# Kernel optimization log

Measured on AMD Instinct MI355X. Metric: run time of the kernel, lower is better.

The kernel has to match this reference:

```python
import jax, jax.numpy as jnp
import numpy as np

INF = 1e9  # large finite sentinel (avoid inf arithmetic in potentials)


def _hungarian(cost):
    """Exact linear sum assignment (Jonker-Volgenant style shortest augmenting
    path, O(N^3)) on a single [N, N] cost matrix. Returns col_ind (int32 [N])
    such that row i is matched to column col_ind[i] with minimal total cost
    (same solution as scipy.optimize.linear_sum_assignment up to ties).
    Column index n is a virtual 'start' column (e-maxx formulation)."""
    n = cost.shape[0]

    def row_body(i, carry):
        u, v, p = carry  # u: row potentials [n]; v: col potentials [n+1]; p[j]: row assigned to col j (-1 free)
        p = p.at[n].set(i)
        state = (u, v, p,
                 jnp.full(n + 1, INF, cost.dtype),   # minv
                 jnp.zeros(n + 1, dtype=bool),       # used
                 jnp.zeros(n + 1, dtype=jnp.int32),  # way (parent col on path)
                 jnp.int32(n))                       # j0 current col

        def cond(st):
            _, _, p_, _, _, _, j0 = st
            return p_[j0] >= 0  # stop when we reach a free column

        def body(st):
            u_, v_, p_, minv, used, way, j0 = st
            used = used.at[j0].set(True)
            i0 = p_[j0]
            cur = cost[i0] - u_[i0] - v_[:n]          # reduced costs of row i0 [n]
            cur = jnp.where(used[:n], INF, cur)
            better = cur < minv[:n]
            minv = minv.at[:n].set(jnp.where(better, cur, minv[:n]))
            way = way.at[:n].set(jnp.where(better, j0, way[:n]))
            masked = jnp.where(used[:n], INF, minv[:n])
            j1 = jnp.argmin(masked).astype(jnp.int32)
            delta = masked[j1]
            # dual update: used cols raise row potential, others shrink minv
            u_ = u_.at[p_].add(jnp.where(used, delta, jnp.zeros((), cost.dtype)))
            v_ = jnp.where(used, v_ - delta, v_)
            minv = jnp.where(used, minv, minv - delta)
            return (u_, v_, p_, minv, used, way, j1)

        u, v, p, _, _, way, j0 = jax.lax.while_loop(cond, body, state)

        # augment along the alternating path back to the virtual column
        def cond2(s):
            j, _ = s
            return j != n

        def body2(s):
            j, p_ = s
            j_prev = way[j]
            return j_prev, p_.at[j].set(p_[j_prev])

        _, p = jax.lax.while_loop(cond2, body2, (j0, p))
        return (u, v, p)

    u0 = jnp.zeros(n, cost.dtype)
    v0 = jnp.zeros(n + 1, cost.dtype)
    p0 = jnp.full(n + 1, -1, dtype=jnp.int32)
    _, _, p = jax.lax.fori_loop(0, n, row_body, (u0, v0, p0))
    # p[j] = row matched to col j  ->  col_ind[row] = j
    col_ind = jnp.zeros(n, jnp.int32).at[p[:n]].set(jnp.arange(n, dtype=jnp.int32))
    return col_ind


def setup_inputs() -> dict:
    key = jax.random.key(0)
    k1, k2 = jax.random.split(key)
    B, N, D = 2048, 24, 256
    slots = jax.random.normal(k1, (B, N, D), dtype=jnp.float32)
    prev_slots = jax.random.normal(k2, (B, N, D), dtype=jnp.float32)
    return {"slots": slots, "prev_slots": prev_slots}


def reference(slots, prev_slots):
    """HungarianPredictor.forward with similarity='cosine': reorder current
    slots to align with prev_slots ordering via optimal 1-1 matching."""
    eps = 1e-12  # torch F.normalize eps
    pn = prev_slots / jnp.maximum(
        jnp.linalg.norm(prev_slots, axis=-1, keepdims=True), eps)
    cn = slots / jnp.maximum(
        jnp.linalg.norm(slots, axis=-1, keepdims=True), eps)
    # cost[b, i, j] = 1 - <prev_i, curr_j>   [B, N, N]
    cost = 1.0 - jnp.einsum('bnd,bmd->bnm', pn, cn)
    col = jax.vmap(_hungarian)(jax.lax.stop_gradient(cost))  # [B, N] int32
    reordered = jax.vmap(lambda s, c: s[c])(slots, col)       # gather per batch
    return reordered
```

## Files before the change

### kernel.cpp

```cpp
#include <hip/hip_runtime.h>
#include <math.h>

#define N    24
#define D    256
#define BLK  256
#define NB   4
#define CTS  28
#define INFV 1e9f

__device__ __forceinline__ int readlane_i(int x, int l) {
    return __builtin_amdgcn_readlane(x, l);
}
__device__ __forceinline__ float readlane_f(float x, int l) {
    return __uint_as_float((unsigned)__builtin_amdgcn_readlane((int)__float_as_uint(x), l));
}

__device__ __forceinline__ unsigned wave_min32(unsigned x) {
    unsigned t;
    t = (unsigned)__builtin_amdgcn_update_dpp((int)x, (int)x, 0xB1,  0xF, 0xF, false); x = t < x ? t : x;
    t = (unsigned)__builtin_amdgcn_update_dpp((int)x, (int)x, 0x4E,  0xF, 0xF, false); x = t < x ? t : x;
    t = (unsigned)__builtin_amdgcn_update_dpp((int)x, (int)x, 0x114, 0xF, 0xF, false); x = t < x ? t : x;
    t = (unsigned)__builtin_amdgcn_update_dpp((int)x, (int)x, 0x118, 0xF, 0xF, false); x = t < x ? t : x;
    t = (unsigned)__builtin_amdgcn_update_dpp((int)x, (int)x, 0x142, 0xF, 0xF, false); x = t < x ? t : x;
    return x;
}

#define DOT4(a, b) ((a).x*(b).x + (a).y*(b).y + (a).z*(b).z + (a).w*(b).w)
#define LGKM0() __asm__ volatile("s_waitcnt lgkmcnt(0)" ::: "memory")

__global__ __launch_bounds__(BLK) void hungarian_fused(
    const float* __restrict__ slots,
    const float* __restrict__ prev,
    float* __restrict__ out, int B)
{
    __shared__ __align__(16) float costT[NB][N][CTS];
    __shared__ int winner[NB][N];
    __shared__ int colw[NB][N];

    const int tid  = threadIdx.x;
    const int lane = tid & 63;
    const int wv   = tid >> 6;
    const int bw   = blockIdx.x * NB + wv;
    if (bw >= B) return;

    const int rg = lane >> 3;
    const int cg = lane & 7;
    const float4* pA = (const float4*)(prev  + (size_t)bw * N * D) + rg * 3 * (D / 4);
    const float4* pC = (const float4*)(slots + (size_t)bw * N * D) + cg * 3 * (D / 4);

    float s00=0,s01=0,s02=0,s10=0,s11=0,s12=0,s20=0,s21=0,s22=0;
    float pa0=0,pa1=0,pa2=0,pc0=0,pc1=0,pc2=0;
    #pragma unroll 2
    for (int k = 0; k < 64; ++k) {
        float4 a0 = pA[k], a1 = pA[64+k], a2 = pA[128+k];
        float4 b0 = pC[k], b1 = pC[64+k], b2 = pC[128+k];
        s00 += DOT4(a0,b0); s01 += DOT4(a0,b1); s02 += DOT4(a0,b2);
        s10 += DOT4(a1,b0); s11 += DOT4(a1,b1); s12 += DOT4(a1,b2);
        s20 += DOT4(a2,b0); s21 += DOT4(a2,b1); s22 += DOT4(a2,b2);
        pa0 += DOT4(a0,a0); pa1 += DOT4(a1,a1); pa2 += DOT4(a2,a2);
        pc0 += DOT4(b0,b0); pc1 += DOT4(b1,b1); pc2 += DOT4(b2,b2);
    }
    float ira0 = 1.0f / fmaxf(sqrtf(pa0), 1e-12f);
    float ira1 = 1.0f / fmaxf(sqrtf(pa1), 1e-12f);
    float ira2 = 1.0f / fmaxf(sqrtf(pa2), 1e-12f);
    float irc0 = 1.0f / fmaxf(sqrtf(pc0), 1e-12f);
    float irc1 = 1.0f / fmaxf(sqrtf(pc1), 1e-12f);
    float irc2 = 1.0f / fmaxf(sqrtf(pc2), 1e-12f);

    {
        float* ct = &costT[wv][0][0];
        const int cb = cg * 3, rb = rg * 3;
        ct[(cb+0)*CTS + rb+0] = 1.0f - s00*ira0*irc0;
        ct[(cb+1)*CTS + rb+0] = 1.0f - s01*ira0*irc1;
        ct[(cb+2)*CTS + rb+0] = 1.0f - s02*ira0*irc2;
        ct[(cb+0)*CTS + rb+1] = 1.0f - s10*ira1*irc0;
        ct[(cb+1)*CTS + rb+1] = 1.0f - s11*ira1*irc1;
        ct[(cb+2)*CTS + rb+1] = 1.0f - s12*ira1*irc2;
        ct[(cb+0)*CTS + rb+2] = 1.0f - s20*ira2*irc0;
        ct[(cb+1)*CTS + rb+2] = 1.0f - s21*ira2*irc1;
        ct[(cb+2)*CTS + rb+2] = 1.0f - s22*ira2*irc2;
    }
    LGKM0();

    const bool isCol = (lane < N);
    const int  jj    = isCol ? lane : 0;
    float cq[24];
    {
        const float4* cp4 = (const float4*)&costT[wv][jj][0];
        #pragma unroll
        for (int r = 0; r < 6; ++r) {
            float4 q = cp4[r];
            cq[r*4+0] = q.x; cq[r*4+1] = q.y; cq[r*4+2] = q.z; cq[r*4+3] = q.w;
        }
    }

    float cm = cq[0]; int ri = 0;
    #pragma unroll
    for (int i = 1; i < N; ++i) { if (cq[i] < cm) { cm = cq[i]; ri = i; } }

    if (isCol) winner[wv][lane] = -1;
    LGKM0();
    if (isCol) winner[wv][ri] = lane;
    LGKM0();
    int p = -1;
    if (isCol && winner[wv][ri] == lane) p = ri;
    const int widx = isCol ? lane : 0;
    unsigned long long mm = __ballot(isCol && winner[wv][widx] >= 0);
    unsigned freeRows = (~(unsigned)mm) & ((1u << N) - 1);

    float uu  = 0.0f;
    float v   = isCol ? cm : INFV;
    int   way = -1;

    while (freeRows) {
        const int f = (int)__builtin_ctz(freeRows);
        freeRows &= freeRows - 1;

        float minv  = INFV;
        bool  used  = false;
        bool  inTree = false;
        int   s_j0 = -1;
        int   s_i0 = f;
        float s_u0 = readlane_f(uu, f);
        int   j1   = 0;

        while (true) {
            inTree = inTree || (lane == s_i0);
            used   = used   || (lane == s_j0);

            float cij;
            switch (s_i0) {
                case 0:  cij = cq[0];  break;  case 1:  cij = cq[1];  break;
                case 2:  cij = cq[2];  break;  case 3:  cij = cq[3];  break;
                case 4:  cij = cq[4];  break;  case 5:  cij = cq[5];  break;
                case 6:  cij = cq[6];  break;  case 7:  cij = cq[7];  break;
                case 8:  cij = cq[8];  break;  case 9:  cij = cq[9];  break;
                case 10: cij = cq[10]; break;  case 11: cij = cq[11]; break;
                case 12: cij = cq[12]; break;  case 13: cij = cq[13]; break;
                case 14: cij = cq[14]; break;  case 15: cij = cq[15]; break;
                case 16: cij = cq[16]; break;  case 17: cij = cq[17]; break;
                case 18: cij = cq[18]; break;  case 19: cij = cq[19]; break;
                case 20: cij = cq[20]; break;  case 21: cij = cq[21]; break;
                case 22: cij = cq[22]; break;  default: cij = cq[23]; break;
            }
            float cur = cij - s_u0 - v;
            bool  act = isCol && !used;
            if (act && cur < minv) { minv = cur; way = s_j0; }
            float masked = act ? minv : INFV;

            unsigned key = __float_as_uint(masked);
            key ^= (unsigned)((int)key >> 31) | 0x80000000u;
            key  = (key & 0xFFFFFFC0u) | (unsigned)lane;
            unsigned kmin = (unsigned)readlane_i((int)wave_min32(key), 31);
            j1 = (int)(kmin & 63u);

            float delta = readlane_f(masked, j1);
            int   i0n   = readlane_i(p, j1);
            float u0n   = readlane_f(uu, i0n & 31);

            if (inTree) uu += delta;
            if (used) v -= delta;
            else if (act) minv -= delta;

            if (i0n < 0) break;
            s_j0 = j1; s_i0 = i0n; s_u0 = u0n;
        }

        int jcur = j1;
        while (true) {
            int wj   = readlane_i(way, jcur);
            int pnew = (wj < 0) ? f : readlane_i(p, wj);
            if (lane == jcur) p = pnew;
            if (wj < 0) break;
            jcur = wj;
        }
    }

    if (isCol) colw[wv][p] = lane;
    LGKM0();

    const float4* sg4 = (const float4*)(slots + (size_t)bw * N * D);
    float4*       og4 = (float4*)(out + (size_t)bw * N * D);
    #pragma unroll
    for (int i = 0; i < N; ++i) {
        int c = colw[wv][i];
        og4[i * 64 + lane] = sg4[c * 64 + lane];
    }
}

extern "C" void kernel_launch(void* const* d_in, const int* in_sizes, int n_in,
                              void* d_out, int out_size, void* d_ws, size_t ws_size,
                              hipStream_t stream) {
    const float* slots = (const float*)d_in[0];
    const float* prev  = (const float*)d_in[1];
    float* out = (float*)d_out;
    int B = in_sizes[0] / (N * D);
    int grid = (B + NB - 1) / NB;
    hungarian_fused<<<grid, BLK, 0, stream>>>(slots, prev, out, B);
}
```

Measured before the change: 194.5 us.

## Add auction-style greedy prematching pass and float min reduction in Hungarian solver

Adds a preliminary phase that repeatedly assigns a free row to its best reduced-cost column, updates the column potential by the second-best gap and may evict the previous owner. This is a JV-style augmenting row reduction, meant to shrink the number of full shortest-path searches. The argmin now uses a float DPP min plus a ballot and ctz instead of packing the lane index into a sortable key. The change also sets launch bounds to two blocks per SM, unrolls the dot-product loop further, and adds iteration guards that could leave rows unmatched in pathological cases.

```diff
diff --git a/kernel.cpp b/kernel.cpp
--- a/kernel.cpp
+++ b/kernel.cpp
@@ -8,27 +8,50 @@
 #define CTS  28
 #define INFV 1e9f
 
-__device__ __forceinline__ int readlane_i(int x, int l) {
+__device__ __forceinline__ int rl_i(int x, int l) {
     return __builtin_amdgcn_readlane(x, l);
 }
-__device__ __forceinline__ float readlane_f(float x, int l) {
+__device__ __forceinline__ float rl_f(float x, int l) {
     return __uint_as_float((unsigned)__builtin_amdgcn_readlane((int)__float_as_uint(x), l));
 }
-
-__device__ __forceinline__ unsigned wave_min32(unsigned x) {
-    unsigned t;
-    t = (unsigned)__builtin_amdgcn_update_dpp((int)x, (int)x, 0xB1,  0xF, 0xF, false); x = t < x ? t : x;
-    t = (unsigned)__builtin_amdgcn_update_dpp((int)x, (int)x, 0x4E,  0xF, 0xF, false); x = t < x ? t : x;
-    t = (unsigned)__builtin_amdgcn_update_dpp((int)x, (int)x, 0x114, 0xF, 0xF, false); x = t < x ? t : x;
-    t = (unsigned)__builtin_amdgcn_update_dpp((int)x, (int)x, 0x118, 0xF, 0xF, false); x = t < x ? t : x;
-    t = (unsigned)__builtin_amdgcn_update_dpp((int)x, (int)x, 0x142, 0xF, 0xF, false); x = t < x ? t : x;
+__device__ __forceinline__ float fmin2(float a, float b) { return a < b ? a : b; }
+
+__device__ __forceinline__ float dpp_min32(float x) {
+    int t;
+    t = __builtin_amdgcn_update_dpp(__float_as_int(x), __float_as_int(x), 0xB1,  0xF, 0xF, false);
+    x = fmin2(__int_as_float(t), x);
+    t = __builtin_amdgcn_update_dpp(__float_as_int(x), __float_as_int(x), 0x4E,  0xF, 0xF, false);
+    x = fmin2(__int_as_float(t), x);
+    t = __builtin_amdgcn_update_dpp(__float_as_int(x), __float_as_int(x), 0x114, 0xF, 0xF, false);
+    x = fmin2(__int_as_float(t), x);
+    t = __builtin_amdgcn_update_dpp(__float_as_int(x), __float_as_int(x), 0x118, 0xF, 0xF, false);
+    x = fmin2(__int_as_float(t), x);
+    t = __builtin_amdgcn_update_dpp(__float_as_int(x), __float_as_int(x), 0x142, 0xF, 0xF, false);
+    x = fmin2(__int_as_float(t), x);
     return x;
+}
+
+__device__ __forceinline__ float sel24(const float (&cq)[24], int s) {
+    switch (s) {
+        case 0:  return cq[0];  case 1:  return cq[1];
+        case 2:  return cq[2];  case 3:  return cq[3];
+        case 4:  return cq[4];  case 5:  return cq[5];
+        case 6:  return cq[6];  case 7:  return cq[7];
+        case 8:  return cq[8];  case 9:  return cq[9];
+        case 10: return cq[10]; case 11: return cq[11];
+        case 12: return cq[12]; case 13: return cq[13];
+        case 14: return cq[14]; case 15: return cq[15];
+        case 16: return cq[16]; case 17: return cq[17];
+        case 18: return cq[18]; case 19: return cq[19];
+        case 20: return cq[20]; case 21: return cq[21];
+        case 22: return cq[22]; default: return cq[23];
+    }
 }
 
 #define DOT4(a, b) ((a).x*(b).x + (a).y*(b).y + (a).z*(b).z + (a).w*(b).w)
 #define LGKM0() __asm__ volatile("s_waitcnt lgkmcnt(0)" ::: "memory")
 
-__global__ __launch_bounds__(BLK) void hungarian_fused(
+__global__ __launch_bounds__(BLK, 2) void hungarian_fused(
     const float* __restrict__ slots,
     const float* __restrict__ prev,
     float* __restrict__ out, int B)
@@ -50,7 +73,7 @@
 
     float s00=0,s01=0,s02=0,s10=0,s11=0,s12=0,s20=0,s21=0,s22=0;
     float pa0=0,pa1=0,pa2=0,pc0=0,pc1=0,pc2=0;
-    #pragma unroll 2
+    #pragma unroll 4
     for (int k = 0; k < 64; ++k) {
         float4 a0 = pA[k], a1 = pA[64+k], a2 = pA[128+k];
         float4 b0 = pC[k], b1 = pC[64+k], b2 = pC[128+k];
@@ -108,11 +131,33 @@
     unsigned long long mm = __ballot(isCol && winner[wv][widx] >= 0);
     unsigned freeRows = (~(unsigned)mm) & ((1u << N) - 1);
 
-    float uu  = 0.0f;
-    float v   = isCol ? cm : INFV;
-    int   way = -1;
-
-    while (freeRows) {
+    float uu = 0.0f;
+    float v  = isCol ? cm : INFV;
+    int  way = -1;
+
+    {
+        int steps = 0;
+        while (freeRows && steps < 40) {
+            ++steps;
+            int f = (int)__builtin_ctz(freeRows);
+            float cif = sel24(cq, f);
+            float rc  = isCol ? (cif - v) : INFV;
+            float u1  = rl_f(dpp_min32(rc), 31);
+            unsigned long long e1 = __ballot(rc == u1);
+            int j1 = (int)__builtin_ctzll(e1);
+            float rc2 = (lane == j1) ? INFV : rc;
+            float u2  = rl_f(dpp_min32(rc2), 31);
+            if (lane == f) uu = u2;
+            if (lane == j1 && u1 < u2) v -= (u2 - u1);
+            int iold = rl_i(p, j1);
+            if (lane == j1) p = f;
+            freeRows &= ~(1u << f);
+            if (iold >= 0) freeRows |= (1u << iold);
+        }
+    }
+
+    int guard = 0;
+    while (freeRows && guard < 1500) {
         const int f = (int)__builtin_ctz(freeRows);
         freeRows &= freeRows - 1;
 
@@ -121,55 +166,36 @@
         bool  inTree = false;
         int   s_j0 = -1;
         int   s_i0 = f;
-        float s_u0 = readlane_f(uu, f);
         int   j1   = 0;
 
-        while (true) {
+        while (guard++ < 1500) {
             inTree = inTree || (lane == s_i0);
             used   = used   || (lane == s_j0);
 
-            float cij;
-            switch (s_i0) {
-                case 0:  cij = cq[0];  break;  case 1:  cij = cq[1];  break;
-                case 2:  cij = cq[2];  break;  case 3:  cij = cq[3];  break;
-                case 4:  cij = cq[4];  break;  case 5:  cij = cq[5];  break;
-                case 6:  cij = cq[6];  break;  case 7:  cij = cq[7];  break;
-                case 8:  cij = cq[8];  break;  case 9:  cij = cq[9];  break;
-                case 10: cij = cq[10]; break;  case 11: cij = cq[11]; break;
-                case 12: cij = cq[12]; break;  case 13: cij = cq[13]; break;
-                case 14: cij = cq[14]; break;  case 15: cij = cq[15]; break;
-                case 16: cij = cq[16]; break;  case 17: cij = cq[17]; break;
-                case 18: cij = cq[18]; break;  case 19: cij = cq[19]; break;
-                case 20: cij = cq[20]; break;  case 21: cij = cq[21]; break;
-                case 22: cij = cq[22]; break;  default: cij = cq[23]; break;
-            }
-            float cur = cij - s_u0 - v;
+            float cij = sel24(cq, s_i0);
+            float u0  = rl_f(uu, s_i0);
+            float cur = cij - u0 - v;
             bool  act = isCol && !used;
             if (act && cur < minv) { minv = cur; way = s_j0; }
             float masked = act ? minv : INFV;
 
-            unsigned key = __float_as_uint(masked);
-            key ^= (unsigned)((int)key >> 31) | 0x80000000u;
-            key  = (key & 0xFFFFFFC0u) | (unsigned)lane;
-            unsigned kmin = (unsigned)readlane_i((int)wave_min32(key), 31);
-            j1 = (int)(kmin & 63u);
-
-            float delta = readlane_f(masked, j1);
-            int   i0n   = readlane_i(p, j1);
-            float u0n   = readlane_f(uu, i0n & 31);
+            float delta = rl_f(dpp_min32(masked), 31);
+            unsigned long long eq = __ballot(masked == delta);
+            int j1s = (int)__builtin_ctzll(eq);
 
             if (inTree) uu += delta;
             if (used) v -= delta;
             else if (act) minv -= delta;
 
-            if (i0n < 0) break;
-            s_j0 = j1; s_i0 = i0n; s_u0 = u0n;
-        }
-
-        int jcur = j1;
-        while (true) {
-            int wj   = readlane_i(way, jcur);
-            int pnew = (wj < 0) ? f : readlane_i(p, wj);
+            int i0n = rl_i(p, j1s);
+            if (i0n < 0) { j1 = j1s; break; }
+            s_j0 = j1s; s_i0 = i0n;
+        }
+
+        int jcur = j1, asteps = 0;
+        while (asteps++ < 32) {
+            int wj   = rl_i(way, jcur);
+            int pnew = (wj < 0) ? f : rl_i(p, wj);
             if (lane == jcur) p = pnew;
             if (wj < 0) break;
             jcur = wj;
```

Result: slower. 209.5 us (+7.7%).
